# Performance work log

Hardware: AMD Instinct MI355X
Metric: run time of the kernel (lower is better)

The kernel has to match this reference:

```python
import jax, jax.numpy as jnp
import numpy as np

HEADS = 16

def _binarize(W):
    # alpha: per-output-row mean of |W| (reduce over all dims except dim 0)
    alpha = jnp.mean(jnp.abs(W), axis=tuple(range(1, W.ndim)), keepdims=True)
    # straight-through sign: forward sign(W), backward identity
    B = W + jax.lax.stop_gradient(jnp.sign(W) - W)
    return alpha * B

def _binlinear(x, W, b):
    Wb = _binarize(W)
    return jnp.einsum('btc,oc->bto', x, Wb) + b

def setup_inputs() -> dict:
    key = jax.random.key(0)
    ks = jax.random.split(key, 9)
    dim = 1024
    B, T = 4, 2048
    inp = {
        'x': jax.random.normal(ks[0], (B, T, dim), jnp.float32),
        'Wq': jax.random.normal(ks[1], (dim, dim), jnp.float32) * 0.02,
        'bq': jax.random.normal(ks[2], (dim,), jnp.float32) * 0.02,
        'Wk': jax.random.normal(ks[3], (dim, dim), jnp.float32) * 0.02,
        'bk': jax.random.normal(ks[4], (dim,), jnp.float32) * 0.02,
        'Wv': jax.random.normal(ks[5], (dim, dim), jnp.float32) * 0.02,
        'bv': jax.random.normal(ks[6], (dim,), jnp.float32) * 0.02,
        'Wp': jax.random.normal(ks[7], (dim, dim), jnp.float32) * 0.02,
        'bp': jax.random.normal(ks[8], (dim,), jnp.float32) * 0.02,
    }
    return inp

def reference(x, Wq, bq, Wk, bk, Wv, bv, Wp, bp):
    B, T, C = x.shape
    H = HEADS
    Dh = C // H
    scale = Dh ** -0.5

    def split_heads(t):
        return t.reshape(B, T, H, Dh).transpose(0, 2, 1, 3)  # [B,H,T,Dh]

    q = split_heads(_binlinear(x, Wq, bq))
    k = split_heads(_binlinear(x, Wk, bk))
    v = split_heads(_binlinear(x, Wv, bv))

    att = jnp.einsum('bhtd,bhsd->bhts', q, k) * scale  # [B,H,T,T]
    att = jax.nn.softmax(att, axis=-1)
    y = jnp.einsum('bhts,bhsd->bhtd', att, v)  # [B,H,T,Dh]
    y = y.transpose(0, 2, 1, 3).reshape(B, T, C)
    return _binlinear(y, Wp, bp)
```

## Files before the change

### kernel.cpp

```cpp
#include <hip/hip_runtime.h>
#include <hip/hip_bf16.h>

typedef short s16x8 __attribute__((ext_vector_type(8)));
typedef float f32x4 __attribute__((ext_vector_type(4)));
typedef unsigned u32x4 __attribute__((ext_vector_type(4)));
typedef unsigned short u16;

#define LOG2E 1.4426950408889634f
#define QSC (0.125f * LOG2E)

typedef __attribute__((address_space(3))) unsigned int lds_u32;
typedef __attribute__((address_space(1))) const unsigned int glb_u32;

static __device__ __forceinline__ void gload16(const void* g, void* l) {
  __builtin_amdgcn_global_load_lds((glb_u32*)g, (lds_u32*)l, 16, 0, 0);
}
static __device__ __forceinline__ u16 bf16u(float f) {
  unsigned u = __builtin_bit_cast(unsigned, f);
  return (u16)((u + 0x7FFFu + ((u >> 16) & 1u)) >> 16);
}
static __device__ __forceinline__ unsigned pk(u16 a, u16 b) {
  return (unsigned)a | ((unsigned)b << 16);
}
static __device__ __forceinline__ unsigned cvtpk(float lo, float hi) {
  unsigned d;
  asm("v_cvt_pk_bf16_f32 %0, %1, %2" : "=v"(d) : "v"(lo), "v"(hi));
  return d;
}
static __device__ __forceinline__ unsigned pk2(float a, float b) {
  float2 f; f.x = a; f.y = b;
  __hip_bfloat162 h = __float22bfloat162_rn(f);
  unsigned r;
  __builtin_memcpy(&r, &h, 4);
  return r;
}

__global__ __launch_bounds__(256) void k_prep(
    const float* __restrict__ x, u16* __restrict__ xb,
    const float* __restrict__ Wq, const float* __restrict__ Wk,
    const float* __restrict__ Wv, const float* __restrict__ Wp,
    const float* __restrict__ bq, const float* __restrict__ bk,
    const float* __restrict__ bv, const float* __restrict__ bp,
    u16* __restrict__ wbqkv, u16* __restrict__ wbp,
    float* __restrict__ alphaf, float* __restrict__ biasf) {
  if (blockIdx.x >= 1024) {
    int i = ((blockIdx.x - 1024) * 256 + threadIdx.x) * 8;
    float4 a = *reinterpret_cast<const float4*>(x + i);
    float4 b = *reinterpret_cast<const float4*>(x + i + 4);
    uint4 w = { pk2(a.x, a.y), pk2(a.z, a.w), pk2(b.x, b.y), pk2(b.z, b.w) };
    *reinterpret_cast<uint4*>(xb + i) = w;
    return;
  }
  int wave = threadIdx.x >> 6, lane = threadIdx.x & 63;
  int row = blockIdx.x * 4 + wave;
  const float* src; const float* bias; int r;
  if (row < 1024)      { src = Wq; bias = bq; r = row; }
  else if (row < 2048) { src = Wk; bias = bk; r = row - 1024; }
  else if (row < 3072) { src = Wv; bias = bv; r = row - 2048; }
  else                 { src = Wp; bias = bp; r = row - 3072; }
  const float4* s4 = reinterpret_cast<const float4*>(src + r * 1024);
  float4 v[4];
  float asum = 0.f;
#pragma unroll
  for (int i = 0; i < 4; ++i) {
    v[i] = s4[lane * 4 + i];
    asum += fabsf(v[i].x) + fabsf(v[i].y) + fabsf(v[i].z) + fabsf(v[i].w);
  }
#pragma unroll
  for (int m = 32; m >= 1; m >>= 1) asum += __shfl_xor(asum, m, 64);
  float alpha = asum * (1.0f / 1024.0f);

  u16 o[16];
#pragma unroll
  for (int i = 0; i < 4; ++i) {
    const float* f = reinterpret_cast<const float*>(&v[i]);
#pragma unroll
    for (int j = 0; j < 4; ++j) {
      float w = f[j];
      o[i * 4 + j] = (w > 0.f) ? (u16)0x3F80 : ((w < 0.f) ? (u16)0xBF80 : (u16)0);
    }
  }
  u16* dst = (row < 3072 ? wbqkv + row * 1024 : wbp + (row - 3072) * 1024) + lane * 16;
  uint4 w0 = { pk(o[0],o[1]), pk(o[2],o[3]), pk(o[4],o[5]), pk(o[6],o[7]) };
  uint4 w1 = { pk(o[8],o[9]), pk(o[10],o[11]), pk(o[12],o[13]), pk(o[14],o[15]) };
  reinterpret_cast<uint4*>(dst)[0] = w0;
  reinterpret_cast<uint4*>(dst)[1] = w1;
  if (lane == 0) {
    float sc = (row < 1024) ? QSC : 1.0f;
    alphaf[row] = alpha * sc;
    biasf[row]  = bias[r] * sc;
  }
}

template <int MODE, int NX, int NWG>
__global__ __launch_bounds__(256) void k_gemm(
    const u16* __restrict__ A, const u16* __restrict__ Bw,
    const float* __restrict__ alphaf, const float* __restrict__ biasf,
    u16* __restrict__ qbuf, u16* __restrict__ kbuf, u16* __restrict__ vtbuf,
    float* __restrict__ outf) {
  __shared__ alignas(128) char smem[65536];
  int tid = threadIdx.x;
  int wave = tid >> 6, l = tid & 63, g = l >> 4, ln = l & 15;
  int wm = (wave >> 1) * 64, wn = (wave & 1) * 64;
  int wg = (blockIdx.x & 7) * (NWG / 8) + (blockIdx.x >> 3);
  int m0 = (wg / NX) * 128, n0 = (wg % NX) * 128;

  f32x4 acc[4][4];
#pragma unroll
  for (int i = 0; i < 4; ++i)
#pragma unroll
    for (int j = 0; j < 4; ++j) acc[i][j] = f32x4{0.f, 0.f, 0.f, 0.f};

  const char* Ab = reinterpret_cast<const char*>(A) + m0 * 2048;
  const char* Bb = reinterpret_cast<const char*>(Bw) + n0 * 2048;

  int soff[4];
#pragma unroll
  for (int i = 0; i < 4; ++i) {
    int P = i * 4096 + tid * 16;
    int r = P >> 7;
    int kc = ((P >> 4) & 7) ^ (r & 7);
    soff[i] = r * 2048 + kc * 16;
  }

#pragma unroll
  for (int i = 0; i < 4; ++i)
    gload16(Ab + soff[i], smem + i * 4096 + wave * 1024);
#pragma unroll
  for (int i = 0; i < 4; ++i)
    gload16(Bb + soff[i], smem + 16384 + i * 4096 + wave * 1024);
  __syncthreads();

  for (int ks = 0; ks < 16; ++ks) {
    int cb = ks & 1;
    if (ks < 15) {
      char* nb = smem + (cb ^ 1) * 32768;
      int kb0 = (ks + 1) * 128;
#pragma unroll
      for (int i = 0; i < 4; ++i)
        gload16(Ab + soff[i] + kb0, nb + i * 4096 + wave * 1024);
#pragma unroll
      for (int i = 0; i < 4; ++i)
        gload16(Bb + soff[i] + kb0, nb + 16384 + i * 4096 + wave * 1024);
    }
    const char* As = smem + cb * 32768;
    const char* Bs = As + 16384;
#pragma unroll
    for (int kk = 0; kk < 2; ++kk) {
      s16x8 af[4], bfr[4];
#pragma unroll
      for (int mf = 0; mf < 4; ++mf) {
        int r = wm + mf * 16 + ln;
        int kb = (kk * 64 + g * 16) ^ ((r & 7) << 4);
        af[mf] = *reinterpret_cast<const s16x8*>(As + r * 128 + kb);
      }
#pragma unroll
      for (int nf = 0; nf < 4; ++nf) {
        int r = wn + nf * 16 + ln;
        int kb = (kk * 64 + g * 16) ^ ((r & 7) << 4);
        bfr[nf] = *reinterpret_cast<const s16x8*>(Bs + r * 128 + kb);
      }
#pragma unroll
      for (int mf = 0; mf < 4; ++mf)
#pragma unroll
        for (int nf = 0; nf < 4; ++nf)
          acc[mf][nf] = __builtin_amdgcn_mfma_f32_16x16x32_bf16(af[mf], bfr[nf], acc[mf][nf], 0, 0, 0);
    }
    __syncthreads();
  }

  if (MODE == 0) {
    if (n0 < 2048) {
      u16* dst = (n0 < 1024) ? qbuf : kbuf;
#pragma unroll
      for (int nf = 0; nf < 4; ++nf) {
        int n = n0 + wn + nf * 16 + ln;
        float al = alphaf[n], bi = biasf[n];
        int nl = n & 1023;
        int h = nl >> 6, d = nl & 63;
#pragma unroll
        for (int mf = 0; mf < 4; ++mf)
#pragma unroll
          for (int rg = 0; rg < 4; ++rg) {
            int m = m0 + wm + mf * 16 + g * 4 + rg;
            int b = m >> 11, t = m & 2047;
            dst[(((b * 16 + h) * 2048 + t) << 6) + d] = bf16u(al * acc[mf][nf][rg] + bi);
          }
      }
    } else {
      u16* ldsT = reinterpret_cast<u16*>(smem);
#pragma unroll
      for (int nf = 0; nf < 4; ++nf) {
        int n = n0 + wn + nf * 16 + ln;
        float al = alphaf[n], bi = biasf[n];
        int nloc = wn + nf * 16 + ln;
#pragma unroll
        for (int mf = 0; mf < 4; ++mf)
#pragma unroll
          for (int rg = 0; rg < 4; ++rg) {
            int mloc = wm + mf * 16 + g * 4 + rg;
            ldsT[mloc * 132 + nloc] = bf16u(al * acc[mf][nf][rg] + bi);
          }
      }
      __syncthreads();
      int dl = tid >> 1;
      int sh = (tid & 1) * 64;
      int nv = n0 - 2048 + dl;
      int h = nv >> 6, d = nv & 63;
      int b = m0 >> 11;
      int s0 = (m0 & 2047) + sh;
      u16* vdst = vtbuf + (((b * 16 + h) * 64 + d) << 11) + s0;
#pragma unroll
      for (int c8 = 0; c8 < 8; ++c8) {
        u16 t0 = ldsT[(sh + c8 * 8 + 0) * 132 + dl], t1 = ldsT[(sh + c8 * 8 + 1) * 132 + dl];
        u16 t2 = ldsT[(sh + c8 * 8 + 2) * 132 + dl], t3 = ldsT[(sh + c8 * 8 + 3) * 132 + dl];
        u16 t4 = ldsT[(sh + c8 * 8 + 4) * 132 + dl], t5 = ldsT[(sh + c8 * 8 + 5) * 132 + dl];
        u16 t6 = ldsT[(sh + c8 * 8 + 6) * 132 + dl], t7 = ldsT[(sh + c8 * 8 + 7) * 132 + dl];
        uint4 w = { pk(t0, t1), pk(t2, t3), pk(t4, t5), pk(t6, t7) };
        *reinterpret_cast<uint4*>(vdst + c8 * 8) = w;
      }
    }
  } else {
#pragma unroll
    for (int nf = 0; nf < 4; ++nf) {
      int n = n0 + wn + nf * 16 + ln;
      float al = alphaf[3072 + n], bi = biasf[3072 + n];
#pragma unroll
      for (int mf = 0; mf < 4; ++mf)
#pragma unroll
        for (int rg = 0; rg < 4; ++rg) {
          int m = m0 + wm + mf * 16 + g * 4 + rg;
          outf[m * 1024 + n] = al * acc[mf][nf][rg] + bi;
        }
    }
  }
}

__global__ __launch_bounds__(512, 4) void k_attn(
    const u16* __restrict__ qb, const u16* __restrict__ kb,
    const u16* __restrict__ vtb, u16* __restrict__ yb) {
  __shared__ alignas(128) char smem[32768];
  int tid = threadIdx.x;
  int wave = tid >> 6, lane = tid & 63;
  int g = lane >> 4, ln = lane & 15;

  int wg = (blockIdx.x & 7) * 64 + (blockIdx.x >> 3);
  int bh = wg >> 3, qt = wg & 7;
  const char* Qg = reinterpret_cast<const char*>(qb) + bh * 262144;
  const char* Kg = reinterpret_cast<const char*>(kb) + bh * 262144;
  const char* Vg = reinterpret_cast<const char*>(vtb) + bh * 262144;

  int qrow = qt * 256 + wave * 32 + ln;
  const s16x8* Qr0 = reinterpret_cast<const s16x8*>(Qg + qrow * 128);
  const s16x8* Qr1 = reinterpret_cast<const s16x8*>(Qg + (qrow + 16) * 128);
  s16x8 qf[2][2];
  qf[0][0] = Qr0[g]; qf[0][1] = Qr0[g + 4];
  qf[1][0] = Qr1[g]; qf[1][1] = Qr1[g + 4];

  s16x8 ones;
#pragma unroll
  for (int i = 0; i < 8; ++i) ones[i] = (short)0x3F80;

  int r = tid >> 3, kc = tid & 7;
  int wr = (r & 3) | (((r >> 3) & 1) << 2);
  int swsrc = (kc ^ wr) * 16;
  int ksrc = r * 128 + swsrc;
  int vsrc = r * 4096 + swsrc;

  int swK = (ln & 7) << 4;
  int swV = ((ln & 3) | (((ln >> 3) & 1) << 2)) << 4;

  f32x4 oacc[2][4];
#pragma unroll
  for (int s = 0; s < 2; ++s)
#pragma unroll
    for (int i = 0; i < 4; ++i) oacc[s][i] = f32x4{0.f, 0.f, 0.f, 0.f};
  f32x4 lacc[2];
  lacc[0] = f32x4{0.f, 0.f, 0.f, 0.f};
  lacc[1] = f32x4{0.f, 0.f, 0.f, 0.f};

  gload16(Kg + ksrc, smem + wave * 1024);
  gload16(Vg + vsrc, smem + 8192 + wave * 1024);
  __syncthreads();

  for (int st = 0; st < 32; ++st) {
    int cb = st & 1;
    if (st < 31) {
      int sb = (st + 1) * 64;
      char* nb = smem + (cb ^ 1) * 16384;
      gload16(Kg + sb * 128 + ksrc, nb + wave * 1024);
      gload16(Vg + sb * 2 + vsrc, nb + 8192 + wave * 1024);
    }
    const char* Kb = smem + cb * 16384;
    const char* Vb = Kb + 8192;

    f32x4 sacc[2][4];
#pragma unroll
    for (int s = 0; s < 2; ++s)
#pragma unroll
      for (int t = 0; t < 4; ++t) sacc[s][t] = f32x4{0.f, 0.f, 0.f, 0.f};
    __builtin_amdgcn_s_setprio(1);
#pragma unroll
    for (int kt = 0; kt < 2; ++kt) {
      int off = (kt * 64 + g * 16) ^ swK;
#pragma unroll
      for (int t = 0; t < 4; ++t) {
        int rho = 32 * (t & 1) + 8 * (ln >> 2) + 4 * (t >> 1) + (ln & 3);
        s16x8 kf = *reinterpret_cast<const s16x8*>(Kb + rho * 128 + off);
        sacc[0][t] = __builtin_amdgcn_mfma_f32_16x16x32_bf16(kf, qf[0][kt], sacc[0][t], 0, 0, 0);
        sacc[1][t] = __builtin_amdgcn_mfma_f32_16x16x32_bf16(kf, qf[1][kt], sacc[1][t], 0, 0, 0);
      }
    }
    __builtin_amdgcn_s_setprio(0);

    s16x8 pf[2][2];
#pragma unroll
    for (int s = 0; s < 2; ++s) {
      float p[4][4];
#pragma unroll
      for (int t = 0; t < 4; ++t)
#pragma unroll
        for (int rg = 0; rg < 4; ++rg)
          p[t][rg] = __builtin_amdgcn_exp2f(sacc[s][t][rg]);
#pragma unroll
      for (int kt = 0; kt < 2; ++kt) {
        u32x4 tw;
        tw[0] = cvtpk(p[kt][0],     p[kt][1]);
        tw[1] = cvtpk(p[kt][2],     p[kt][3]);
        tw[2] = cvtpk(p[kt + 2][0], p[kt + 2][1]);
        tw[3] = cvtpk(p[kt + 2][2], p[kt + 2][3]);
        pf[s][kt] = __builtin_bit_cast(s16x8, tw);
      }
    }

#pragma unroll
    for (int s = 0; s < 2; ++s)
#pragma unroll
      for (int kt = 0; kt < 2; ++kt)
        lacc[s] = __builtin_amdgcn_mfma_f32_16x16x32_bf16(ones, pf[s][kt], lacc[s], 0, 0, 0);

    __builtin_amdgcn_s_setprio(1);
#pragma unroll
    for (int kt = 0; kt < 2; ++kt) {
      int off = (kt * 64 + g * 16) ^ swV;
#pragma unroll
      for (int dt = 0; dt < 4; ++dt) {
        s16x8 vf = *reinterpret_cast<const s16x8*>(Vb + (dt * 16 + ln) * 128 + off);
        oacc[0][dt] = __builtin_amdgcn_mfma_f32_16x16x32_bf16(vf, pf[0][kt], oacc[0][dt], 0, 0, 0);
        oacc[1][dt] = __builtin_amdgcn_mfma_f32_16x16x32_bf16(vf, pf[1][kt], oacc[1][dt], 0, 0, 0);
      }
    }
    __builtin_amdgcn_s_setprio(0);
    __syncthreads();
  }

  int b = bh >> 4, h = bh & 15;
#pragma unroll
  for (int s = 0; s < 2; ++s) {
    float linv = 1.0f / lacc[s][0];
    u16* yrow = yb + (b * 2048 + qrow + s * 16) * 1024 + h * 64;
#pragma unroll
    for (int dt = 0; dt < 4; ++dt) {
      uint2 w;
      w.x = cvtpk(oacc[s][dt][0] * linv, oacc[s][dt][1] * linv);
      w.y = cvtpk(oacc[s][dt][2] * linv, oacc[s][dt][3] * linv);
      *reinterpret_cast<uint2*>(yrow + dt * 16 + g * 4) = w;
    }
  }
}

extern "C" void kernel_launch(void* const* d_in, const int* in_sizes, int n_in,
                              void* d_out, int out_size, void* d_ws, size_t ws_size,
                              hipStream_t stream) {
  (void)in_sizes; (void)n_in; (void)out_size; (void)ws_size;
  const float* x  = (const float*)d_in[0];
  const float* Wq = (const float*)d_in[1];
  const float* bq = (const float*)d_in[2];
  const float* Wk = (const float*)d_in[3];
  const float* bk = (const float*)d_in[4];
  const float* Wv = (const float*)d_in[5];
  const float* bv = (const float*)d_in[6];
  const float* Wp = (const float*)d_in[7];
  const float* bp = (const float*)d_in[8];

  char* ws = (char*)d_ws;
  u16*   xb    = (u16*)(ws);
  u16*   wbqkv = (u16*)(ws + 16777216);
  u16*   wbp   = (u16*)(ws + 23068672);
  float* alphaf = (float*)(ws + 25165824);
  float* biasf  = (float*)(ws + 25182208);
  u16*   vtbuf = (u16*)(ws + 25198592);
  u16*   ybuf  = xb;
  u16*   qbuf  = (u16*)d_out;
  u16*   kbuf  = (u16*)d_out + 8388608;
  float* outf  = (float*)d_out;

  k_prep<<<5120, 256, 0, stream>>>(x, xb, Wq, Wk, Wv, Wp, bq, bk, bv, bp, wbqkv, wbp, alphaf, biasf);
  k_gemm<0, 24, 1536><<<1536, 256, 0, stream>>>(xb, wbqkv, alphaf, biasf, qbuf, kbuf, vtbuf, nullptr);
  k_attn<<<512, 512, 0, stream>>>(qbuf, kbuf, vtbuf, ybuf);
  k_gemm<1, 8, 512><<<512, 256, 0, stream>>>(ybuf, wbp, alphaf, biasf, nullptr, nullptr, nullptr, outf);
}
```

Before: 154.2 us.

## Double attention KV tile to 128 keys and process in 32-key chunks

```diff
diff --git a/kernel.cpp b/kernel.cpp
--- a/kernel.cpp
+++ b/kernel.cpp
@@ -239,7 +239,7 @@
 __global__ __launch_bounds__(512, 4) void k_attn(
     const u16* __restrict__ qb, const u16* __restrict__ kb,
     const u16* __restrict__ vtb, u16* __restrict__ yb) {
-  __shared__ alignas(128) char smem[32768];
+  __shared__ alignas(128) char smem[65536];
   int tid = threadIdx.x;
   int wave = tid >> 6, lane = tid & 63;
   int g = lane >> 4, ln = lane & 15;
@@ -261,11 +261,17 @@
 #pragma unroll
   for (int i = 0; i < 8; ++i) ones[i] = (short)0x3F80;
 
-  int r = tid >> 3, kc = tid & 7;
-  int wr = (r & 3) | (((r >> 3) & 1) << 2);
-  int swsrc = (kc ^ wr) * 16;
-  int ksrc = r * 128 + swsrc;
-  int vsrc = r * 4096 + swsrc;
+  int ksrc[2], vsrc[2];
+#pragma unroll
+  for (int i = 0; i < 2; ++i) {
+    int P = i * 8192 + tid * 16;
+    int rk = P >> 7, kck = (P >> 4) & 7;
+    int wk = (rk & 3) | (((rk >> 3) & 1) << 2);
+    ksrc[i] = rk * 128 + (kck ^ wk) * 16;
+    int rv = P >> 8, kcv = (P >> 4) & 15;
+    int wv = (rv & 3) | (((rv >> 3) & 1) << 2);
+    vsrc[i] = rv * 4096 + (kcv ^ wv) * 16;
+  }
 
   int swK = (ln & 7) << 4;
   int swV = ((ln & 3) | (((ln >> 3) & 1) << 2)) << 4;
@@ -279,78 +285,82 @@
   lacc[0] = f32x4{0.f, 0.f, 0.f, 0.f};
   lacc[1] = f32x4{0.f, 0.f, 0.f, 0.f};
 
-  gload16(Kg + ksrc, smem + wave * 1024);
-  gload16(Vg + vsrc, smem + 8192 + wave * 1024);
+#pragma unroll
+  for (int i = 0; i < 2; ++i) {
+    gload16(Kg + ksrc[i], smem + i * 8192 + wave * 1024);
+    gload16(Vg + vsrc[i], smem + 32768 + i * 8192 + wave * 1024);
+  }
   __syncthreads();
 
-  for (int st = 0; st < 32; ++st) {
+  for (int st = 0; st < 16; ++st) {
     int cb = st & 1;
-    if (st < 31) {
-      int sb = (st + 1) * 64;
-      char* nb = smem + (cb ^ 1) * 16384;
-      gload16(Kg + sb * 128 + ksrc, nb + wave * 1024);
-      gload16(Vg + sb * 2 + vsrc, nb + 8192 + wave * 1024);
+    if (st < 15) {
+      char* nk = smem + (cb ^ 1) * 16384;
+      char* nv = smem + 32768 + (cb ^ 1) * 16384;
+      const char* gk = Kg + (st + 1) * 16384;
+      const char* gv = Vg + (st + 1) * 256;
+#pragma unroll
+      for (int i = 0; i < 2; ++i) {
+        gload16(gk + ksrc[i], nk + i * 8192 + wave * 1024);
+        gload16(gv + vsrc[i], nv + i * 8192 + wave * 1024);
+      }
     }
     const char* Kb = smem + cb * 16384;
-    const char* Vb = Kb + 8192;
-
-    f32x4 sacc[2][4];
-#pragma unroll
-    for (int s = 0; s < 2; ++s)
-#pragma unroll
-      for (int t = 0; t < 4; ++t) sacc[s][t] = f32x4{0.f, 0.f, 0.f, 0.f};
-    __builtin_amdgcn_s_setprio(1);
-#pragma unroll
-    for (int kt = 0; kt < 2; ++kt) {
-      int off = (kt * 64 + g * 16) ^ swK;
-#pragma unroll
-      for (int t = 0; t < 4; ++t) {
-        int rho = 32 * (t & 1) + 8 * (ln >> 2) + 4 * (t >> 1) + (ln & 3);
-        s16x8 kf = *reinterpret_cast<const s16x8*>(Kb + rho * 128 + off);
-        sacc[0][t] = __builtin_amdgcn_mfma_f32_16x16x32_bf16(kf, qf[0][kt], sacc[0][t], 0, 0, 0);
-        sacc[1][t] = __builtin_amdgcn_mfma_f32_16x16x32_bf16(kf, qf[1][kt], sacc[1][t], 0, 0, 0);
-      }
-    }
-    __builtin_amdgcn_s_setprio(0);
-
-    s16x8 pf[2][2];
-#pragma unroll
-    for (int s = 0; s < 2; ++s) {
-      float p[4][4];
-#pragma unroll
-      for (int t = 0; t < 4; ++t)
-#pragma unroll
-        for (int rg = 0; rg < 4; ++rg)
-          p[t][rg] = __builtin_amdgcn_exp2f(sacc[s][t][rg]);
+    const char* Vb = smem + 32768 + cb * 16384;
+
+#pragma unroll
+    for (int c = 0; c < 4; ++c) {
+      f32x4 sa[2][2];
+#pragma unroll
+      for (int s = 0; s < 2; ++s)
+#pragma unroll
+        for (int h = 0; h < 2; ++h) sa[s][h] = f32x4{0.f, 0.f, 0.f, 0.f};
+      int rho0 = 32 * c + 8 * (ln >> 2) + (ln & 3);
+      __builtin_amdgcn_s_setprio(1);
 #pragma unroll
       for (int kt = 0; kt < 2; ++kt) {
+        int off = (kt * 64 + g * 16) ^ swK;
+        s16x8 kf0 = *reinterpret_cast<const s16x8*>(Kb + rho0 * 128 + off);
+        s16x8 kf1 = *reinterpret_cast<const s16x8*>(Kb + (rho0 + 4) * 128 + off);
+        sa[0][0] = __builtin_amdgcn_mfma_f32_16x16x32_bf16(kf0, qf[0][kt], sa[0][0], 0, 0, 0);
+        sa[1][0] = __builtin_amdgcn_mfma_f32_16x16x32_bf16(kf0, qf[1][kt], sa[1][0], 0, 0, 0);
+        sa[0][1] = __builtin_amdgcn_mfma_f32_16x16x32_bf16(kf1, qf[0][kt], sa[0][1], 0, 0, 0);
+        sa[1][1] = __builtin_amdgcn_mfma_f32_16x16x32_bf16(kf1, qf[1][kt], sa[1][1], 0, 0, 0);
+      }
+      __builtin_amdgcn_s_setprio(0);
+
+      s16x8 pf[2];
+#pragma unroll
+      for (int s = 0; s < 2; ++s) {
+        float p0 = __builtin_amdgcn_exp2f(sa[s][0][0]);
+        float p1 = __builtin_amdgcn_exp2f(sa[s][0][1]);
+        float p2 = __builtin_amdgcn_exp2f(sa[s][0][2]);
+        float p3 = __builtin_amdgcn_exp2f(sa[s][0][3]);
+        float p4 = __builtin_amdgcn_exp2f(sa[s][1][0]);
+        float p5 = __builtin_amdgcn_exp2f(sa[s][1][1]);
+        float p6 = __builtin_amdgcn_exp2f(sa[s][1][2]);
+        float p7 = __builtin_amdgcn_exp2f(sa[s][1][3]);
         u32x4 tw;
-        tw[0] = cvtpk(p[kt][0],     p[kt][1]);
-        tw[1] = cvtpk(p[kt][2],     p[kt][3]);
-        tw[2] = cvtpk(p[kt + 2][0], p[kt + 2][1]);
-        tw[3] = cvtpk(p[kt + 2][2], p[kt + 2][3]);
-        pf[s][kt] = __builtin_bit_cast(s16x8, tw);
-      }
-    }
-
-#pragma unroll
-    for (int s = 0; s < 2; ++s)
-#pragma unroll
-      for (int kt = 0; kt < 2; ++kt)
-        lacc[s] = __builtin_amdgcn_mfma_f32_16x16x32_bf16(ones, pf[s][kt], lacc[s], 0, 0, 0);
-
-    __builtin_amdgcn_s_setprio(1);
-#pragma unroll
-    for (int kt = 0; kt < 2; ++kt) {
-      int off = (kt * 64 + g * 16) ^ swV;
+        tw[0] = cvtpk(p0, p1);
+        tw[1] = cvtpk(p2, p3);
+        tw[2] = cvtpk(p4, p5);
+        tw[3] = cvtpk(p6, p7);
+        pf[s] = __builtin_bit_cast(s16x8, tw);
+      }
+
+      lacc[0] = __builtin_amdgcn_mfma_f32_16x16x32_bf16(ones, pf[0], lacc[0], 0, 0, 0);
+      lacc[1] = __builtin_amdgcn_mfma_f32_16x16x32_bf16(ones, pf[1], lacc[1], 0, 0, 0);
+
+      int offv = (c * 64 + g * 16) ^ swV;
+      __builtin_amdgcn_s_setprio(1);
 #pragma unroll
       for (int dt = 0; dt < 4; ++dt) {
-        s16x8 vf = *reinterpret_cast<const s16x8*>(Vb + (dt * 16 + ln) * 128 + off);
-        oacc[0][dt] = __builtin_amdgcn_mfma_f32_16x16x32_bf16(vf, pf[0][kt], oacc[0][dt], 0, 0, 0);
-        oacc[1][dt] = __builtin_amdgcn_mfma_f32_16x16x32_bf16(vf, pf[1][kt], oacc[1][dt], 0, 0, 0);
-      }
-    }
-    __builtin_amdgcn_s_setprio(0);
+        s16x8 vf = *reinterpret_cast<const s16x8*>(Vb + (dt * 16 + ln) * 256 + offv);
+        oacc[0][dt] = __builtin_amdgcn_mfma_f32_16x16x32_bf16(vf, pf[0], oacc[0][dt], 0, 0, 0);
+        oacc[1][dt] = __builtin_amdgcn_mfma_f32_16x16x32_bf16(vf, pf[1], oacc[1][dt], 0, 0, 0);
+      }
+      __builtin_amdgcn_s_setprio(0);
+    }
     __syncthreads();
   }
 
```

Measured after the change: 154.1 us. Within noise of the previous version (-0.1%).

## Add 256x256-tile 8-wave QKV GEMM with interleaved staging and MFMA phases

Applied to the files above, without the earlier changes.

```diff
diff --git a/kernel.cpp b/kernel.cpp
--- a/kernel.cpp
+++ b/kernel.cpp
@@ -92,6 +92,210 @@
   }
 }
 
+template <int NX, int NWG>
+__global__ __launch_bounds__(512, 2) void k_gemm8(
+    const u16* __restrict__ A, const u16* __restrict__ Bw,
+    const float* __restrict__ alphaf, const float* __restrict__ biasf,
+    u16* __restrict__ qbuf, u16* __restrict__ kbuf, u16* __restrict__ vtbuf) {
+  __shared__ alignas(128) char smem[131072];
+  int tid = threadIdx.x;
+  int wave = tid >> 6, lane = tid & 63, g = lane >> 4, ln = lane & 15;
+  int wq = wave >> 2;
+  int wr = wave & 3;
+  int wg = (blockIdx.x & 7) * (NWG / 8) + (blockIdx.x >> 3);
+  int m0 = (wg / NX) * 256, n0 = (wg % NX) * 256;
+
+  f32x4 acc[8][4];
+#pragma unroll
+  for (int i = 0; i < 8; ++i)
+#pragma unroll
+    for (int j = 0; j < 4; ++j) acc[i][j] = f32x4{0.f, 0.f, 0.f, 0.f};
+
+  const char* Ab = reinterpret_cast<const char*>(A) + m0 * 2048;
+  const char* Bb = reinterpret_cast<const char*>(Bw) + n0 * 2048;
+  const char* Asrc[2] = { Ab, Ab + 262144 };
+  const char* Bsrc[2] = { Bb, Bb + 262144 };
+
+  int soff[2], ldst[2];
+#pragma unroll
+  for (int i = 0; i < 2; ++i) {
+    int r = i * 64 + (tid >> 3);
+    int kc = tid & 7;
+    soff[i] = r * 2048 + (kc ^ (r & 7)) * 16;
+    ldst[i] = i * 8192 + wave * 1024;
+  }
+
+#define HT(buf, hid) (smem + (buf) * 65536 + (hid) * 16384)
+#define STG(buf, hid, srcb, kt)                                              \
+  {                                                                          \
+    _Pragma("unroll")                                                        \
+    for (int i_ = 0; i_ < 2; ++i_)                                           \
+      gload16((srcb) + (kt) * 128 + soff[i_], HT(buf, hid) + ldst[i_]);      \
+  }
+
+  s16x8 areg[4][2], breg[2][2];
+#define READA(ah, buf)                                                       \
+  {                                                                          \
+    _Pragma("unroll")                                                        \
+    for (int mfl_ = 0; mfl_ < 4; ++mfl_) {                                   \
+      int r_ = wq * 64 + mfl_ * 16 + ln;                                     \
+      _Pragma("unroll")                                                      \
+      for (int kk_ = 0; kk_ < 2; ++kk_)                                      \
+        areg[mfl_][kk_] = *reinterpret_cast<const s16x8*>(                   \
+            HT(buf, ah) + r_ * 128 + ((kk_ * 64 + g * 16) ^ ((r_ & 7) << 4)));\
+    }                                                                        \
+  }
+#define READB(bh, buf)                                                       \
+  {                                                                          \
+    _Pragma("unroll")                                                        \
+    for (int nfl_ = 0; nfl_ < 2; ++nfl_) {                                   \
+      int r_ = wr * 32 + nfl_ * 16 + ln;                                     \
+      _Pragma("unroll")                                                      \
+      for (int kk_ = 0; kk_ < 2; ++kk_)                                      \
+        breg[nfl_][kk_] = *reinterpret_cast<const s16x8*>(                   \
+            HT(buf, 2 + (bh)) + r_ * 128 + ((kk_ * 64 + g * 16) ^ ((r_ & 7) << 4)));\
+    }                                                                        \
+  }
+#define MFMA16(ah, bh)                                                       \
+  {                                                                          \
+    __builtin_amdgcn_s_setprio(1);                                           \
+    _Pragma("unroll")                                                        \
+    for (int kk_ = 0; kk_ < 2; ++kk_)                                        \
+      _Pragma("unroll")                                                      \
+      for (int mfl_ = 0; mfl_ < 4; ++mfl_)                                   \
+        _Pragma("unroll")                                                    \
+        for (int nfl_ = 0; nfl_ < 2; ++nfl_)                                 \
+          acc[(ah) * 4 + mfl_][(bh) * 2 + nfl_] =                            \
+              __builtin_amdgcn_mfma_f32_16x16x32_bf16(                       \
+                  areg[mfl_][kk_], breg[nfl_][kk_],                          \
+                  acc[(ah) * 4 + mfl_][(bh) * 2 + nfl_], 0, 0, 0);           \
+    __builtin_amdgcn_s_setprio(0);                                           \
+  }
+#define BAR1()                                                               \
+  __builtin_amdgcn_sched_barrier(0);                                         \
+  __builtin_amdgcn_s_barrier();                                              \
+  asm volatile("s_waitcnt lgkmcnt(0)" ::: "memory");                         \
+  __builtin_amdgcn_sched_barrier(0);
+#define BAR2()                                                               \
+  __builtin_amdgcn_sched_barrier(0);                                         \
+  __builtin_amdgcn_s_barrier();
+#define VMW(n)                                                               \
+  asm volatile("s_waitcnt vmcnt(" #n ")" ::: "memory");                      \
+  __builtin_amdgcn_sched_barrier(0);
+
+  STG(0, 0, Asrc[0], 0); STG(0, 1, Asrc[1], 0);
+  STG(0, 2, Bsrc[0], 0); STG(0, 3, Bsrc[1], 0);
+  STG(1, 0, Asrc[0], 1); STG(1, 3, Bsrc[1], 1);
+  VMW(4);
+  __builtin_amdgcn_s_barrier();
+
+  for (int it = 0; it < 8; ++it) {
+    int t2 = 2 * it + 2, t3 = 2 * it + 3;
+    bool nl = (it < 7);
+    READA(0, 0); READB(0, 0);
+    STG(1, 1, Asrc[1], 2 * it + 1);
+    BAR1(); MFMA16(0, 0); BAR2();
+    READB(1, 0);
+    STG(1, 2, Bsrc[0], 2 * it + 1);
+    BAR1(); MFMA16(0, 1); BAR2();
+    READA(1, 0);
+    if (nl) STG(0, 0, Asrc[0], t2);
+    BAR1(); MFMA16(1, 1); BAR2();
+    READB(0, 0);
+    if (nl) STG(0, 3, Bsrc[1], t2);
+    BAR1(); MFMA16(1, 0);
+    if (nl) { VMW(4); } else { VMW(0); }
+    BAR2();
+    READA(0, 1); READB(0, 1);
+    if (nl) STG(0, 1, Asrc[1], t2);
+    BAR1(); MFMA16(0, 0); BAR2();
+    READB(1, 1);
+    if (nl) STG(0, 2, Bsrc[0], t2);
+    BAR1(); MFMA16(0, 1); BAR2();
+    READA(1, 1);
+    if (nl) STG(1, 0, Asrc[0], t3);
+    BAR1(); MFMA16(1, 1); BAR2();
+    READB(0, 1);
+    if (nl) STG(1, 3, Bsrc[1], t3);
+    BAR1(); MFMA16(1, 0);
+    if (nl) { VMW(4); }
+    BAR2();
+  }
+
+  if (n0 < 2048) {
+    u16* dst = (n0 < 1024) ? qbuf : kbuf;
+#pragma unroll
+    for (int bh = 0; bh < 2; ++bh)
+#pragma unroll
+      for (int nfl = 0; nfl < 2; ++nfl) {
+        int n = n0 + bh * 128 + wr * 32 + nfl * 16 + ln;
+        float al = alphaf[n], bi = biasf[n];
+        int nl2 = n & 1023;
+        int h = nl2 >> 6, d = nl2 & 63;
+#pragma unroll
+        for (int ah = 0; ah < 2; ++ah)
+#pragma unroll
+          for (int mfl = 0; mfl < 4; ++mfl)
+#pragma unroll
+            for (int rg = 0; rg < 4; ++rg) {
+              int m = m0 + ah * 128 + wq * 64 + mfl * 16 + g * 4 + rg;
+              int b = m >> 11, t = m & 2047;
+              dst[(((b * 16 + h) * 2048 + t) << 6) + d] =
+                  bf16u(al * acc[ah * 4 + mfl][bh * 2 + nfl][rg] + bi);
+            }
+      }
+  } else {
+    u16* ldsT = reinterpret_cast<u16*>(smem);
+    int b = m0 >> 11;
+#pragma unroll
+    for (int mh = 0; mh < 2; ++mh) {
+      __syncthreads();
+#pragma unroll
+      for (int bh = 0; bh < 2; ++bh)
+#pragma unroll
+        for (int nfl = 0; nfl < 2; ++nfl) {
+          int n = n0 + bh * 128 + wr * 32 + nfl * 16 + ln;
+          float al = alphaf[n], bi = biasf[n];
+          int nloc = bh * 128 + wr * 32 + nfl * 16 + ln;
+#pragma unroll
+          for (int mfl = 0; mfl < 4; ++mfl)
+#pragma unroll
+            for (int rg = 0; rg < 4; ++rg) {
+              int mloc = wq * 64 + mfl * 16 + g * 4 + rg;
+              ldsT[mloc * 260 + nloc] =
+                  bf16u(al * acc[mh * 4 + mfl][bh * 2 + nfl][rg] + bi);
+            }
+        }
+      __syncthreads();
+      int dl = tid >> 1;
+      int sh = (tid & 1) * 64;
+      int nv = n0 - 2048 + dl;
+      int h = nv >> 6, d = nv & 63;
+      int s0 = (m0 & 2047) + mh * 128 + sh;
+      u16* vdst = vtbuf + (((b * 16 + h) * 64 + d) << 11) + s0;
+#pragma unroll
+      for (int c8 = 0; c8 < 8; ++c8) {
+        u16 t0 = ldsT[(sh + c8 * 8 + 0 - sh) * 260 + dl + (sh + c8 * 8) * 0];
+        (void)t0;
+        u16 e0 = ldsT[(sh + c8 * 8 + 0) * 260 + dl], e1 = ldsT[(sh + c8 * 8 + 1) * 260 + dl];
+        u16 e2 = ldsT[(sh + c8 * 8 + 2) * 260 + dl], e3 = ldsT[(sh + c8 * 8 + 3) * 260 + dl];
+        u16 e4 = ldsT[(sh + c8 * 8 + 4) * 260 + dl], e5 = ldsT[(sh + c8 * 8 + 5) * 260 + dl];
+        u16 e6 = ldsT[(sh + c8 * 8 + 6) * 260 + dl], e7 = ldsT[(sh + c8 * 8 + 7) * 260 + dl];
+        uint4 w = { pk(e0, e1), pk(e2, e3), pk(e4, e5), pk(e6, e7) };
+        *reinterpret_cast<uint4*>(vdst + c8 * 8) = w;
+      }
+    }
+  }
+#undef HT
+#undef STG
+#undef READA
+#undef READB
+#undef MFMA16
+#undef BAR1
+#undef BAR2
+#undef VMW
+}
+
 template <int MODE, int NX, int NWG>
 __global__ __launch_bounds__(256) void k_gemm(
     const u16* __restrict__ A, const u16* __restrict__ Bw,
@@ -170,56 +374,6 @@
   }
 
   if (MODE == 0) {
-    if (n0 < 2048) {
-      u16* dst = (n0 < 1024) ? qbuf : kbuf;
-#pragma unroll
-      for (int nf = 0; nf < 4; ++nf) {
-        int n = n0 + wn + nf * 16 + ln;
-        float al = alphaf[n], bi = biasf[n];
-        int nl = n & 1023;
-        int h = nl >> 6, d = nl & 63;
-#pragma unroll
-        for (int mf = 0; mf < 4; ++mf)
-#pragma unroll
-          for (int rg = 0; rg < 4; ++rg) {
-            int m = m0 + wm + mf * 16 + g * 4 + rg;
-            int b = m >> 11, t = m & 2047;
-            dst[(((b * 16 + h) * 2048 + t) << 6) + d] = bf16u(al * acc[mf][nf][rg] + bi);
-          }
-      }
-    } else {
-      u16* ldsT = reinterpret_cast<u16*>(smem);
-#pragma unroll
-      for (int nf = 0; nf < 4; ++nf) {
-        int n = n0 + wn + nf * 16 + ln;
-        float al = alphaf[n], bi = biasf[n];
-        int nloc = wn + nf * 16 + ln;
-#pragma unroll
-        for (int mf = 0; mf < 4; ++mf)
-#pragma unroll
-          for (int rg = 0; rg < 4; ++rg) {
-            int mloc = wm + mf * 16 + g * 4 + rg;
-            ldsT[mloc * 132 + nloc] = bf16u(al * acc[mf][nf][rg] + bi);
-          }
-      }
-      __syncthreads();
-      int dl = tid >> 1;
-      int sh = (tid & 1) * 64;
-      int nv = n0 - 2048 + dl;
-      int h = nv >> 6, d = nv & 63;
-      int b = m0 >> 11;
-      int s0 = (m0 & 2047) + sh;
-      u16* vdst = vtbuf + (((b * 16 + h) * 64 + d) << 11) + s0;
-#pragma unroll
-      for (int c8 = 0; c8 < 8; ++c8) {
-        u16 t0 = ldsT[(sh + c8 * 8 + 0) * 132 + dl], t1 = ldsT[(sh + c8 * 8 + 1) * 132 + dl];
-        u16 t2 = ldsT[(sh + c8 * 8 + 2) * 132 + dl], t3 = ldsT[(sh + c8 * 8 + 3) * 132 + dl];
-        u16 t4 = ldsT[(sh + c8 * 8 + 4) * 132 + dl], t5 = ldsT[(sh + c8 * 8 + 5) * 132 + dl];
-        u16 t6 = ldsT[(sh + c8 * 8 + 6) * 132 + dl], t7 = ldsT[(sh + c8 * 8 + 7) * 132 + dl];
-        uint4 w = { pk(t0, t1), pk(t2, t3), pk(t4, t5), pk(t6, t7) };
-        *reinterpret_cast<uint4*>(vdst + c8 * 8) = w;
-      }
-    }
   } else {
 #pragma unroll
     for (int nf = 0; nf < 4; ++nf) {
@@ -262,8 +416,8 @@
   for (int i = 0; i < 8; ++i) ones[i] = (short)0x3F80;
 
   int r = tid >> 3, kc = tid & 7;
-  int wr = (r & 3) | (((r >> 3) & 1) << 2);
-  int swsrc = (kc ^ wr) * 16;
+  int wr2 = (r & 3) | (((r >> 3) & 1) << 2);
+  int swsrc = (kc ^ wr2) * 16;
   int ksrc = r * 128 + swsrc;
   int vsrc = r * 4096 + swsrc;
 
@@ -396,7 +550,7 @@
   float* outf  = (float*)d_out;
 
   k_prep<<<5120, 256, 0, stream>>>(x, xb, Wq, Wk, Wv, Wp, bq, bk, bv, bp, wbqkv, wbp, alphaf, biasf);
-  k_gemm<0, 24, 1536><<<1536, 256, 0, stream>>>(xb, wbqkv, alphaf, biasf, qbuf, kbuf, vtbuf, nullptr);
+  k_gemm8<12, 384><<<384, 512, 0, stream>>>(xb, wbqkv, alphaf, biasf, qbuf, kbuf, vtbuf);
   k_attn<<<512, 512, 0, stream>>>(qbuf, kbuf, vtbuf, ybuf);
   k_gemm<1, 8, 512><<<512, 256, 0, stream>>>(ybuf, wbp, alphaf, biasf, nullptr, nullptr, nullptr, outf);
 }
```

After: 160.0 us. 3.7% more time.
